# Kernel tuning notes

Measured on AMD Instinct MI355X. Metric: run time of the kernel, lower is better.

Reference implementation:

```python
import jax, jax.numpy as jnp
import numpy as np

N_NODES = 20000
N_EDGES = 320000
EMB = 128


def setup_inputs() -> dict:
    key = jax.random.key(0)
    ks = jax.random.split(key, 8)
    h = jax.random.normal(ks[0], (N_NODES, EMB), dtype=jnp.float32)
    W1 = jax.random.normal(ks[1], (2 * EMB, 4 * EMB), dtype=jnp.float32) / np.sqrt(2 * EMB)
    b1 = jnp.zeros((4 * EMB,), dtype=jnp.float32)
    W2 = jax.random.normal(ks[2], (4 * EMB, 1), dtype=jnp.float32) / np.sqrt(4 * EMB)
    b2 = jnp.zeros((1,), dtype=jnp.float32)
    # logistic-noise uniforms for RelaxedBernoulli rsample, kept away from {0,1}
    u = jax.random.uniform(ks[3], (N_EDGES,), dtype=jnp.float32, minval=1e-6, maxval=1.0 - 1e-6)
    row = jax.random.randint(ks[4], (N_EDGES,), 0, N_NODES, dtype=jnp.int32)
    col = jax.random.randint(ks[5], (N_EDGES,), 0, N_NODES, dtype=jnp.int32)
    edge_mask = -jnp.ones((N_EDGES,), dtype=jnp.int32)  # torch code initializes mask to -1
    return {"h": h, "W1": W1, "b1": b1, "W2": W2, "b2": b2,
            "u": u, "row": row, "col": col, "edge_mask": edge_mask, "hierarchy": 0}


def _segment_softmax(scores, seg, num_segments):
    m = jax.ops.segment_max(scores, seg, num_segments=num_segments)
    e = jnp.exp(scores - m[seg])
    s = jax.ops.segment_sum(e, seg, num_segments=num_segments)
    return e / s[seg]


TEMPERATURE = 1.0
RATIO = 0.5  # threshold for hard bernoulli


def reference(h, W1, b1, W2, b2, u, row, col, edge_mask, hierarchy):
    # edge gather + concat: [E, 2*EMB]
    edge_rep = jnp.concatenate([h[row], h[col]], axis=-1)
    # 2-layer MLP edge scorer -> [E]
    hid = jax.nn.relu(edge_rep @ W1 + b1)
    scores = (hid @ W2 + b2).reshape(-1)
    # segment softmax over edges grouped by source node (torch: softmax(edge_score, edge_index[0]))
    probs = _segment_softmax(scores, row, N_NODES)
    # RelaxedBernoulli(temperature, probs).rsample(): sigmoid((logits + logistic)/T)
    logits = jnp.log(probs) - jnp.log1p(-probs)
    logistic = jnp.log(u) - jnp.log1p(-u)
    y = jax.nn.sigmoid((logits + logistic) / TEMPERATURE)
    y_hard = (y > RATIO).astype(y.dtype)
    y_st = jax.lax.stop_gradient(y_hard - y) + y  # straight-through
    # edge_mask[y == 1] = hierarchy + 1
    new_mask = jnp.where(y_st == 1.0, jnp.int32(hierarchy + 1), edge_mask)
    c_idx = new_mask > 0
    s_idx = new_mask == -1
    causal_w = jnp.where(c_idx, scores, 0.0)
    spu_w = jnp.where(s_idx, -scores, 0.0)
    return scores, y_st, new_mask, causal_w, spu_w
```

## Files before the change

kernel.cpp:

```cpp
#include <hip/hip_runtime.h>
#include <math.h>

#define N_NODES 20000
#define N_EDGES 320000
#define EMB 128
#define HID 512
#define NCHUNK ((N_NODES + 1023) / 1024)

#define RPW 4
#define WPB 2
#define RPB (RPW * WPB)
#define FE_BLOCKS ((N_NODES + RPB - 1) / RPB)

typedef float v2f __attribute__((ext_vector_type(2)));

#if defined(__has_builtin)
#if __has_builtin(__builtin_elementwise_fma)
#define V2FMA(a, b, c) __builtin_elementwise_fma((a), (b), (c))
#else
#define V2FMA(a, b, c) ((a) * (b) + (c))
#endif
#else
#define V2FMA(a, b, c) ((a) * (b) + (c))
#endif

__global__ void init_deg(int* __restrict__ deg, int* __restrict__ offs) {
    int i = blockIdx.x * 256 + threadIdx.x;
    if (i < N_NODES) deg[i] = 0;
    if (i == 0) offs[N_NODES] = N_EDGES;
}

#define TM 128
#define TN 128
#define BK 8
#define NTILES (EMB / BK)
#define GEMM_MT ((N_NODES + TM - 1) / TM)
#define GEMM_BLOCKS (8 * GEMM_MT)
#define HIST_BLOCKS ((N_EDGES + 255) / 256)

__global__ __launch_bounds__(256) void gemm_hist(
    const float* __restrict__ h, const float* __restrict__ W1,
    const float* __restrict__ b1, float* __restrict__ P, float* __restrict__ Q,
    const int* __restrict__ row, int* __restrict__ deg)
{
    const int bid = blockIdx.x;
    const int tid = threadIdx.x;

    if (bid >= GEMM_BLOCKS) {
        const int e = (bid - GEMM_BLOCKS) * 256 + tid;
        if (e < N_EDGES) atomicAdd(&deg[row[e]], 1);
        return;
    }

    __shared__ float As[2][BK][TM + 4];
    __shared__ float Bs[2][BK][TN];

    const int nt = bid & 7;
    const int mt = bid >> 3;
    const int m_base = mt * TM;

    const int a_m = tid >> 1;
    const int a_k = (tid & 1) << 2;
    const int  row_a = m_base + a_m;
    const bool a_ok  = row_a < N_NODES;
    const float* __restrict__ hrow = h + (size_t)row_a * EMB + a_k;

    const int b_k = tid >> 5;
    const int b_n = (tid & 31) << 2;
    const int w_row_off = (nt < 4) ? 0 : 128;
    const int w_col     = (nt & 3) * TN + b_n;
    const float* __restrict__ wrow = W1 + (size_t)(w_row_off + b_k) * HID + w_col;

    const int ty = tid >> 4, tx = tid & 15;
    const int cm = ty << 2, cn = tx << 2;

    v2f acc[8][4] = {};

    float4 pa, pb;
    pa = make_float4(0.f, 0.f, 0.f, 0.f);
    if (a_ok) pa = *(const float4*)(hrow);
    pb = *(const float4*)(wrow);
    As[0][a_k + 0][a_m] = pa.x;
    As[0][a_k + 1][a_m] = pa.y;
    As[0][a_k + 2][a_m] = pa.z;
    As[0][a_k + 3][a_m] = pa.w;
    *(float4*)&Bs[0][b_k][b_n] = pb;
    __syncthreads();

    for (int t = 0; t < NTILES; ++t) {
        const int cur = t & 1;
        if (t + 1 < NTILES) {
            const int k0 = (t + 1) * BK;
            pa = make_float4(0.f, 0.f, 0.f, 0.f);
            if (a_ok) pa = *(const float4*)(hrow + k0);
            pb = *(const float4*)(wrow + (size_t)k0 * HID);
        }

#pragma unroll
        for (int kk = 0; kk < BK; ++kk) {
            float a[8];
            *(float4*)&a[0] = *(const float4*)&As[cur][kk][cm];
            *(float4*)&a[4] = *(const float4*)&As[cur][kk][cm + 64];
            float4 b0 = *(const float4*)&Bs[cur][kk][cn];
            float4 b1v = *(const float4*)&Bs[cur][kk][cn + 64];
            v2f bp[4] = {(v2f){b0.x, b0.y}, (v2f){b0.z, b0.w},
                         (v2f){b1v.x, b1v.y}, (v2f){b1v.z, b1v.w}};
#pragma unroll
            for (int i = 0; i < 8; ++i) {
                v2f ai = (v2f){a[i], a[i]};
#pragma unroll
                for (int j = 0; j < 4; ++j)
                    acc[i][j] = V2FMA(ai, bp[j], acc[i][j]);
            }
        }

        if (t + 1 < NTILES) {
            const int nxt = 1 - cur;
            As[nxt][a_k + 0][a_m] = pa.x;
            As[nxt][a_k + 1][a_m] = pa.y;
            As[nxt][a_k + 2][a_m] = pa.z;
            As[nxt][a_k + 3][a_m] = pa.w;
            *(float4*)&Bs[nxt][b_k][b_n] = pb;
            __syncthreads();
        }
    }

    const bool  isP = (nt < 4);
    const int   col_base = (nt & 3) * TN;
    float* __restrict__ dstbase = isP ? P : Q;

    v2f bias[4] = {{0.f,0.f},{0.f,0.f},{0.f,0.f},{0.f,0.f}};
    if (isP) {
        float4 bv0 = *(const float4*)(b1 + col_base + cn);
        float4 bv1 = *(const float4*)(b1 + col_base + cn + 64);
        bias[0] = (v2f){bv0.x, bv0.y};
        bias[1] = (v2f){bv0.z, bv0.w};
        bias[2] = (v2f){bv1.x, bv1.y};
        bias[3] = (v2f){bv1.z, bv1.w};
    }

#pragma unroll
    for (int i = 0; i < 8; ++i) {
        const int r = m_base + cm + (i < 4 ? i : 64 + i - 4);
        if (r < N_NODES) {
            float* dst = dstbase + (size_t)r * HID + col_base;
            v2f c0 = acc[i][0] + bias[0], c1 = acc[i][1] + bias[1];
            v2f c2 = acc[i][2] + bias[2], c3 = acc[i][3] + bias[3];
            *(float4*)(dst + cn)      = make_float4(c0.x, c0.y, c1.x, c1.y);
            *(float4*)(dst + cn + 64) = make_float4(c2.x, c2.y, c3.x, c3.y);
        }
    }
}

__device__ __forceinline__ int wave_incl_scan(int v, int lane) {
#pragma unroll
    for (int off = 1; off < 64; off <<= 1) {
        int t = __shfl_up(v, off, 64);
        if (lane >= off) v += t;
    }
    return v;
}

__global__ __launch_bounds__(1024) void scan_part(const int* __restrict__ deg,
                                                  int* __restrict__ part,
                                                  int* __restrict__ totals) {
    __shared__ int wsum[16];
    const int tid = threadIdx.x, lane = tid & 63, w = tid >> 6;
    const int i = blockIdx.x * 1024 + tid;
    int v = (i < N_NODES) ? deg[i] : 0;
    int incl = wave_incl_scan(v, lane);
    if (lane == 63) wsum[w] = incl;
    __syncthreads();
    if (w == 0) {
        int x = (lane < 16) ? wsum[lane] : 0;
        int xs = wave_incl_scan(x, lane);
        if (lane < 16) wsum[lane] = xs - x;
        if (lane == 15) totals[blockIdx.x] = xs;
    }
    __syncthreads();
    if (i < N_NODES) part[i] = wsum[w] + incl - v;
}

__global__ __launch_bounds__(1024) void scan_apply(const int* __restrict__ part,
                                                   const int* __restrict__ totals,
                                                   int* __restrict__ cursor,
                                                   int* __restrict__ offs) {
    __shared__ int carry_s;
    const int tid = threadIdx.x;
    if (tid < 64) {
        int v = (tid < NCHUNK) ? totals[tid] : 0;
        int incl = wave_incl_scan(v, tid);
        if (tid == (int)blockIdx.x) carry_s = incl - v;
    }
    __syncthreads();
    const int i = blockIdx.x * 1024 + tid;
    if (i < N_NODES) {
        int o = part[i] + carry_s;
        cursor[i] = o;
        offs[i] = o;
    }
}

__global__ void scatter_edges(const int* __restrict__ row, const int* __restrict__ col,
                              int* __restrict__ cursor,
                              unsigned short* __restrict__ cols16,
                              int* __restrict__ inv) {
    int e = blockIdx.x * 256 + threadIdx.x;
    if (e >= N_EDGES) return;
    int r = row[e];
    int pos = atomicAdd(&cursor[r], 1);
    cols16[pos] = (unsigned short)col[e];
    inv[e] = pos;
}

__device__ __forceinline__ float dot8_relu(const float4 qa, const float4 qb,
                                           const float4 p0, const float4 p1,
                                           const float4 w0, const float4 w1) {
    float t = 0.0f;
    t = fmaf(fmaxf(p0.x + qa.x, 0.0f), w0.x, t);
    t = fmaf(fmaxf(p0.y + qa.y, 0.0f), w0.y, t);
    t = fmaf(fmaxf(p0.z + qa.z, 0.0f), w0.z, t);
    t = fmaf(fmaxf(p0.w + qa.w, 0.0f), w0.w, t);
    t = fmaf(fmaxf(p1.x + qb.x, 0.0f), w1.x, t);
    t = fmaf(fmaxf(p1.y + qb.y, 0.0f), w1.y, t);
    t = fmaf(fmaxf(p1.z + qb.z, 0.0f), w1.z, t);
    t = fmaf(fmaxf(p1.w + qb.w, 0.0f), w1.w, t);
    return t;
}

__device__ __forceinline__ float chunk_scores(
    const float* __restrict__ Q, const unsigned short* __restrict__ cols16,
    int es_base, int nch, int lane, int j0,
    const float4 p0, const float4 p1, const float4 w0, const float4 w1,
    float bias2)
{
    int mycol = 0;
    if (lane < nch) mycol = (int)cols16[es_base + lane];
    float mysc = -INFINITY;

#define QL2(k, bb, d0, d1) { \
        int c_ = __shfl(mycol, (bb) + (k), 64); \
        const float* __restrict__ q_ = Q + (size_t)c_ * HID; \
        d0 = *(const float4*)(q_ + j0); \
        d1 = *(const float4*)(q_ + 256 + j0); }

    float4 a00, a01, a10, a11;
    QL2(0, 0, a00, a01); QL2(1, 0, a10, a11);

    for (int b = 0; b < nch; b += 2) {
        float4 n00, n01, n10, n11;
        const bool more = (b + 2) < nch;
        if (more) { QL2(0, b + 2, n00, n01); QL2(1, b + 2, n10, n11); }

        float s0 = dot8_relu(a00, a01, p0, p1, w0, w1);
        float s1 = dot8_relu(a10, a11, p0, p1, w0, w1);

#pragma unroll
        for (int off = 32; off > 0; off >>= 1) {
            s0 += __shfl_xor(s0, off, 64);
            s1 += __shfl_xor(s1, off, 64);
        }

        const int k = lane - b;
        if ((unsigned)k < 2u && lane < nch) mysc = (k ? s1 : s0) + bias2;

        if (more) { a00 = n00; a01 = n01; a10 = n10; a11 = n11; }
    }
#undef QL2
    return mysc;
}

__global__ __launch_bounds__(128) void fused_edge(
    const float* __restrict__ P, const float* __restrict__ Q,
    const float* __restrict__ W2, const float* __restrict__ b2,
    const unsigned short* __restrict__ cols16, const int* __restrict__ offs,
    float2* __restrict__ tmp)
{
    const int tid = threadIdx.x, lane = tid & 63, w = tid >> 6;
    const int r0 = blockIdx.x * RPB + w * RPW;
    const int r1 = (r0 + RPW < N_NODES) ? r0 + RPW : N_NODES;
    const int j0 = lane << 2;

    const float4 w0 = *(const float4*)(W2 + j0);
    const float4 w1 = *(const float4*)(W2 + 256 + j0);
    const float bias2 = b2[0];

    for (int r = r0; r < r1; ++r) {
        const int es = offs[r], ee = offs[r + 1];
        const int d = ee - es;
        if (d == 0) continue;

        const float* __restrict__ prow = P + (size_t)r * HID;
        const float4 p0 = *(const float4*)(prow + j0);
        const float4 p1 = *(const float4*)(prow + 256 + j0);

        if (d <= 64) {
            float mysc = chunk_scores(Q, cols16, es, d, lane, j0,
                                      p0, p1, w0, w1, bias2);

            float m = mysc;
#pragma unroll
            for (int off = 32; off > 0; off >>= 1)
                m = fmaxf(m, __shfl_xor(m, off, 64));

            float ev = (lane < d) ? expf(mysc - m) : 0.0f;
            float ssum = ev;
#pragma unroll
            for (int off = 32; off > 0; off >>= 1)
                ssum += __shfl_xor(ssum, off, 64);

            if (lane < d) {
                float p = ev / ssum;
                float logits = logf(p) - log1pf(-p);
                tmp[es + lane] = make_float2(mysc, logits);
            }
        } else {
            for (int base = 0; base < d; base += 64) {
                const int nch = (d - base < 64) ? d - base : 64;
                float mysc = chunk_scores(Q, cols16, es + base, nch, lane, j0,
                                          p0, p1, w0, w1, bias2);
                if (lane < nch) tmp[es + base + lane].x = mysc;
            }

            float m = -INFINITY;
            for (int j = lane; j < d; j += 64)
                m = fmaxf(m, tmp[es + j].x);
#pragma unroll
            for (int off = 32; off > 0; off >>= 1)
                m = fmaxf(m, __shfl_xor(m, off, 64));

            float ssum = 0.0f;
            for (int j = lane; j < d; j += 64)
                ssum += expf(tmp[es + j].x - m);
#pragma unroll
            for (int off = 32; off > 0; off >>= 1)
                ssum += __shfl_xor(ssum, off, 64);

            for (int j = lane; j < d; j += 64) {
                float s = tmp[es + j].x;
                float p = expf(s - m) / ssum;
                float logits = logf(p) - log1pf(-p);
                tmp[es + j] = make_float2(s, logits);
            }
        }
    }
}

__global__ __launch_bounds__(256) void unperm(
    const float2* __restrict__ tmp, const int* __restrict__ inv,
    const float* __restrict__ u, const int* __restrict__ edge_mask,
    const int* __restrict__ hierarchy,
    float* __restrict__ scores, float* __restrict__ out_y,
    float* __restrict__ out_mask, float* __restrict__ out_causal,
    float* __restrict__ out_spu)
{
    const int e = blockIdx.x * 256 + threadIdx.x;
    if (e >= N_EDGES) return;
    const float2 t = tmp[inv[e]];
    const float s = t.x;
    const float uu = u[e];
    const float L = logf(uu) - log1pf(-uu);
    const float y = 1.0f / (1.0f + expf(-(t.y + L)));
    const bool hard = y > 0.5f;
    const int mm = hard ? (hierarchy[0] + 1) : edge_mask[e];
    scores[e]     = s;
    out_y[e]      = hard ? 1.0f : 0.0f;
    out_mask[e]   = (float)mm;
    out_causal[e] = (mm > 0)   ?  s : 0.0f;
    out_spu[e]    = (mm == -1) ? -s : 0.0f;
}

extern "C" void kernel_launch(void* const* d_in, const int* in_sizes, int n_in,
                              void* d_out, int out_size, void* d_ws, size_t ws_size,
                              hipStream_t stream) {
    const float* h_ptr = (const float*)d_in[0];
    const float* W1    = (const float*)d_in[1];
    const float* b1    = (const float*)d_in[2];
    const float* W2    = (const float*)d_in[3];
    const float* b2    = (const float*)d_in[4];
    const float* u     = (const float*)d_in[5];
    const int*   row   = (const int*)d_in[6];
    const int*   col   = (const int*)d_in[7];
    const int*   emask = (const int*)d_in[8];
    const int*   hier  = (const int*)d_in[9];

    float* out        = (float*)d_out;
    float* scores     = out;
    float* out_y      = out + (size_t)N_EDGES;
    float* out_mask   = out + 2 * (size_t)N_EDGES;
    float* out_causal = out + 3 * (size_t)N_EDGES;
    float* out_spu    = out + 4 * (size_t)N_EDGES;

    float*          P      = (float*)d_ws;
    float*          Qm     = P + (size_t)N_NODES * HID;
    float2*         tmp    = (float2*)(Qm + (size_t)N_NODES * HID);
    unsigned short* cols16 = (unsigned short*)(tmp + N_EDGES);
    int*            inv    = (int*)(cols16 + N_EDGES);
    int*            deg    = inv + N_EDGES;
    int*            cursor = deg + N_NODES;
    int*            offs   = cursor + N_NODES;
    int*            part   = offs + N_NODES + 1;
    int*            totals = part + N_NODES;

    hipLaunchKernelGGL(init_deg, dim3((N_NODES + 255) / 256), dim3(256), 0, stream,
                       deg, offs);

    hipLaunchKernelGGL(gemm_hist, dim3(GEMM_BLOCKS + HIST_BLOCKS), dim3(256), 0, stream,
                       h_ptr, W1, b1, P, Qm, row, deg);

    hipLaunchKernelGGL(scan_part, dim3(NCHUNK), dim3(1024), 0, stream, deg, part, totals);
    hipLaunchKernelGGL(scan_apply, dim3(NCHUNK), dim3(1024), 0, stream,
                       part, totals, cursor, offs);
    hipLaunchKernelGGL(scatter_edges, dim3((N_EDGES + 255) / 256), dim3(256), 0, stream,
                       row, col, cursor, cols16, inv);

    hipLaunchKernelGGL(fused_edge, dim3(FE_BLOCKS), dim3(128), 0, stream,
                       P, Qm, W2, b2, cols16, offs, tmp);

    hipLaunchKernelGGL(unperm, dim3((N_EDGES + 255) / 256), dim3(256), 0, stream,
                       tmp, inv, u, emask, hier,
                       scores, out_y, out_mask, out_causal, out_spu);
}
```

Baseline: 275.6 us.

## Stream Q rows through an LDS ring via async global_load_lds across rows

Replaces the register double-buffered per-row chunk_scores with a per-wave 4-slot LDS ring filled by global_load_lds. Prefetches run continuously across the wave's rows instead of restarting at each row. Waits are handled with manual s_waitcnt vmcnt counts, and edges are scored one per iteration instead of two. The aim is to hide Q-gather latency across row boundaries. The risks are correctness of the hand-tuned vmcnt accounting, given other outstanding loads such as P and cols16, and lower instruction-level parallelism per iteration.

Measured after the change: 316.7 us. 14.9% more time.

```diff
diff --git a/kernel.cpp b/kernel.cpp
--- a/kernel.cpp
+++ b/kernel.cpp
@@ -11,6 +11,7 @@
 #define WPB 2
 #define RPB (RPW * WPB)
 #define FE_BLOCKS ((N_NODES + RPB - 1) / RPB)
+#define SLOTS 4
 
 typedef float v2f __attribute__((ext_vector_type(2)));
 
@@ -23,6 +24,14 @@
 #else
 #define V2FMA(a, b, c) ((a) * (b) + (c))
 #endif
+
+#define WAITVM(N) asm volatile("s_waitcnt vmcnt(" #N ")" ::: "memory")
+
+__device__ __forceinline__ void stage16(const float* g, float* l) {
+    __builtin_amdgcn_global_load_lds(
+        (const __attribute__((address_space(1))) void*)g,
+        (__attribute__((address_space(3))) void*)l, 16, 0, 0);
+}
 
 __global__ void init_deg(int* __restrict__ deg, int* __restrict__ offs) {
     int i = blockIdx.x * 256 + threadIdx.x;
@@ -135,6 +144,8 @@
         float4 bv1 = *(const float4*)(b1 + col_base + cn + 64);
         bias[0] = (v2f){bv0.x, bv0.y};
         bias[1] = (v2f){bv0.z, bv0.w};
+        bias[2] = (v2f){bv1.x, bv1.y};
+        bias[3] = (v2f){bv1.w == bv1.w ? bv1.x : bv1.x, bv1.y};
         bias[2] = (v2f){bv1.x, bv1.y};
         bias[3] = (v2f){bv1.z, bv1.w};
     }
@@ -228,76 +239,102 @@
     return t;
 }
 
-__device__ __forceinline__ float chunk_scores(
-    const float* __restrict__ Q, const unsigned short* __restrict__ cols16,
-    int es_base, int nch, int lane, int j0,
-    const float4 p0, const float4 p1, const float4 w0, const float4 w1,
-    float bias2)
-{
-    int mycol = 0;
-    if (lane < nch) mycol = (int)cols16[es_base + lane];
-    float mysc = -INFINITY;
-
-#define QL2(k, bb, d0, d1) { \
-        int c_ = __shfl(mycol, (bb) + (k), 64); \
-        const float* __restrict__ q_ = Q + (size_t)c_ * HID; \
-        d0 = *(const float4*)(q_ + j0); \
-        d1 = *(const float4*)(q_ + 256 + j0); }
-
-    float4 a00, a01, a10, a11;
-    QL2(0, 0, a00, a01); QL2(1, 0, a10, a11);
-
-    for (int b = 0; b < nch; b += 2) {
-        float4 n00, n01, n10, n11;
-        const bool more = (b + 2) < nch;
-        if (more) { QL2(0, b + 2, n00, n01); QL2(1, b + 2, n10, n11); }
-
-        float s0 = dot8_relu(a00, a01, p0, p1, w0, w1);
-        float s1 = dot8_relu(a10, a11, p0, p1, w0, w1);
-
-#pragma unroll
-        for (int off = 32; off > 0; off >>= 1) {
-            s0 += __shfl_xor(s0, off, 64);
-            s1 += __shfl_xor(s1, off, 64);
-        }
-
-        const int k = lane - b;
-        if ((unsigned)k < 2u && lane < nch) mysc = (k ? s1 : s0) + bias2;
-
-        if (more) { a00 = n00; a01 = n01; a10 = n10; a11 = n11; }
-    }
-#undef QL2
-    return mysc;
-}
-
 __global__ __launch_bounds__(128) void fused_edge(
     const float* __restrict__ P, const float* __restrict__ Q,
     const float* __restrict__ W2, const float* __restrict__ b2,
     const unsigned short* __restrict__ cols16, const int* __restrict__ offs,
     float2* __restrict__ tmp)
 {
+    __shared__ float ring[WPB][SLOTS][HID];
+
     const int tid = threadIdx.x, lane = tid & 63, w = tid >> 6;
     const int r0 = blockIdx.x * RPB + w * RPW;
-    const int r1 = (r0 + RPW < N_NODES) ? r0 + RPW : N_NODES;
+    if (r0 >= N_NODES) return;
+    const int nrow = (r0 + RPW <= N_NODES) ? RPW : (N_NODES - r0);
     const int j0 = lane << 2;
+
+    int o[RPW + 1];
+#pragma unroll
+    for (int t = 0; t <= RPW; ++t)
+        o[t] = offs[r0 + ((t <= nrow) ? t : nrow)];
+
+    const int es0 = o[0];
+    const int n = o[nrow] - es0;
+    if (n == 0) return;
 
     const float4 w0 = *(const float4*)(W2 + j0);
     const float4 w1 = *(const float4*)(W2 + 256 + j0);
     const float bias2 = b2[0];
 
-    for (int r = r0; r < r1; ++r) {
-        const int es = offs[r], ee = offs[r + 1];
-        const int d = ee - es;
+    int cb = 0;
+    int mc0 = 0, mc1 = 0;
+    if (lane < n) mc0 = (int)cols16[es0 + lane];
+    if (n > 64 && 64 + lane < n) mc1 = (int)cols16[es0 + 64 + lane];
+
+    const int pro = (n < SLOTS) ? n : SLOTS;
+    for (int jj = 0; jj < pro; ++jj) {
+        int c = __shfl(mc0, jj, 64);
+        const float* qs = Q + (size_t)c * HID;
+        stage16(qs + j0,       &ring[w][jj][0]);
+        stage16(qs + 256 + j0, &ring[w][jj][256]);
+    }
+
+    int i = 0;
+    for (int rr = 0; rr < nrow; ++rr) {
+        const int d = o[rr + 1] - o[rr];
         if (d == 0) continue;
-
+        const int r = r0 + rr;
         const float* __restrict__ prow = P + (size_t)r * HID;
         const float4 p0 = *(const float4*)(prow + j0);
         const float4 p1 = *(const float4*)(prow + 256 + j0);
 
+        const int es_r = es0 + i;
+        float mysc = -INFINITY;
+
+        for (int k = 0; k < d; ++k, ++i) {
+            if ((i >> 6) > cb) {
+                cb++;
+                mc0 = mc1;
+                mc1 = 0;
+                const int base = (cb + 1) << 6;
+                if (base < n && base + lane < n)
+                    mc1 = (int)cols16[es0 + base + lane];
+            }
+
+            const int rem = n - 1 - i;
+            if (rem >= 3)      { WAITVM(6); }
+            else if (rem == 2) { WAITVM(4); }
+            else if (rem == 1) { WAITVM(2); }
+            else               { WAITVM(0); }
+
+            const int sl = i & (SLOTS - 1);
+            const float4 q0 = *(const float4*)&ring[w][sl][j0];
+            const float4 q1 = *(const float4*)&ring[w][sl][256 + j0];
+
+            float s = dot8_relu(q0, q1, p0, p1, w0, w1);
+#pragma unroll
+            for (int off = 32; off > 0; off >>= 1)
+                s += __shfl_xor(s, off, 64);
+            const int kk = k & 63;
+            if (lane == kk) mysc = s + bias2;
+
+            if (kk == 63 && k != d - 1) {
+                tmp[es_r + (k - 63) + lane].x = mysc;
+                mysc = -INFINITY;
+            }
+
+            const int j = i + SLOTS;
+            if (j < n) {
+                const int mcsel = ((j >> 6) == cb) ? mc0 : mc1;
+                const int c = __shfl(mcsel, j & 63, 64);
+                const float* qs = Q + (size_t)c * HID;
+                const int s2 = j & (SLOTS - 1);
+                stage16(qs + j0,       &ring[w][s2][0]);
+                stage16(qs + 256 + j0, &ring[w][s2][256]);
+            }
+        }
+
         if (d <= 64) {
-            float mysc = chunk_scores(Q, cols16, es, d, lane, j0,
-                                      p0, p1, w0, w1, bias2);
-
             float m = mysc;
 #pragma unroll
             for (int off = 32; off > 0; off >>= 1)
@@ -312,35 +349,32 @@
             if (lane < d) {
                 float p = ev / ssum;
                 float logits = logf(p) - log1pf(-p);
-                tmp[es + lane] = make_float2(mysc, logits);
+                tmp[es_r + lane] = make_float2(mysc, logits);
             }
         } else {
-            for (int base = 0; base < d; base += 64) {
-                const int nch = (d - base < 64) ? d - base : 64;
-                float mysc = chunk_scores(Q, cols16, es + base, nch, lane, j0,
-                                          p0, p1, w0, w1, bias2);
-                if (lane < nch) tmp[es + base + lane].x = mysc;
-            }
+            const int last_base = ((d - 1) >> 6) << 6;
+            const int cnt = d - last_base;
+            if (lane < cnt) tmp[es_r + last_base + lane].x = mysc;
 
             float m = -INFINITY;
-            for (int j = lane; j < d; j += 64)
-                m = fmaxf(m, tmp[es + j].x);
+            for (int jj = lane; jj < d; jj += 64)
+                m = fmaxf(m, tmp[es_r + jj].x);
 #pragma unroll
             for (int off = 32; off > 0; off >>= 1)
                 m = fmaxf(m, __shfl_xor(m, off, 64));
 
             float ssum = 0.0f;
-            for (int j = lane; j < d; j += 64)
-                ssum += expf(tmp[es + j].x - m);
+            for (int jj = lane; jj < d; jj += 64)
+                ssum += expf(tmp[es_r + jj].x - m);
 #pragma unroll
             for (int off = 32; off > 0; off >>= 1)
                 ssum += __shfl_xor(ssum, off, 64);
 
-            for (int j = lane; j < d; j += 64) {
-                float s = tmp[es + j].x;
-                float p = expf(s - m) / ssum;
+            for (int jj = lane; jj < d; jj += 64) {
+                float sv = tmp[es_r + jj].x;
+                float p = expf(sv - m) / ssum;
                 float logits = logf(p) - log1pf(-p);
-                tmp[es + j] = make_float2(s, logits);
+                tmp[es_r + jj] = make_float2(sv, logits);
             }
         }
     }
```

## Replace FP32 FMA node GEMM with split-bf16 MFMA matrix-core GEMM

Applied to the files above, without the earlier changes.

Converts h and W1 into three-term bf16 splits in a prep kernel that also runs the degree histogram. A new GEMM then computes the P/Q node projections with 16x16x32 bf16 MFMA instructions, using six cross products to approximate FP32 accuracy. The goal is to move the per-node projection GEMM from vector FMA units onto matrix cores. In exchange it adds an extra kernel launch, writes and reads the bf16 split buffers, loads operands straight from global memory with no LDS tiling, and carries a small precision risk from dropping the lower-order split terms.

Result: slower. 330.1 us (+19.8%).

```diff
diff --git a/kernel.cpp b/kernel.cpp
--- a/kernel.cpp
+++ b/kernel.cpp
@@ -12,17 +12,19 @@
 #define RPB (RPW * WPB)
 #define FE_BLOCKS ((N_NODES + RPB - 1) / RPB)
 
-typedef float v2f __attribute__((ext_vector_type(2)));
-
-#if defined(__has_builtin)
-#if __has_builtin(__builtin_elementwise_fma)
-#define V2FMA(a, b, c) __builtin_elementwise_fma((a), (b), (c))
-#else
-#define V2FMA(a, b, c) ((a) * (b) + (c))
-#endif
-#else
-#define V2FMA(a, b, c) ((a) * (b) + (c))
-#endif
+#define GEMM_MT ((N_NODES + 127) / 128)
+#define GEMM_MFMA_BLOCKS (GEMM_MT * 8)
+
+#define PREP_H_BLOCKS 2500
+#define PREP_W_BLOCKS 512
+#define HIST_BLOCKS ((N_EDGES + 255) / 256)
+#define PREP_HIST_OFF (PREP_H_BLOCKS + PREP_W_BLOCKS)
+#define PREP_BLOCKS (PREP_HIST_OFF + HIST_BLOCKS)
+
+typedef __attribute__((ext_vector_type(8))) short bf16x8;
+typedef __attribute__((ext_vector_type(4))) float f32x4;
+
+#define MFMA16(a, b, c) __builtin_amdgcn_mfma_f32_16x16x32_bf16((a), (b), (c), 0, 0, 0)
 
 __global__ void init_deg(int* __restrict__ deg, int* __restrict__ offs) {
     int i = blockIdx.x * 256 + threadIdx.x;
@@ -30,124 +32,139 @@
     if (i == 0) offs[N_NODES] = N_EDGES;
 }
 
-#define TM 128
-#define TN 128
-#define BK 8
-#define NTILES (EMB / BK)
-#define GEMM_MT ((N_NODES + TM - 1) / TM)
-#define GEMM_BLOCKS (8 * GEMM_MT)
-#define HIST_BLOCKS ((N_EDGES + 255) / 256)
-
-__global__ __launch_bounds__(256) void gemm_hist(
+__device__ __forceinline__ unsigned short bf16rn(float x) {
+    unsigned u = __builtin_bit_cast(unsigned, x);
+    u += 0x7FFFu + ((u >> 16) & 1u);
+    return (unsigned short)(u >> 16);
+}
+__device__ __forceinline__ float bf2f(unsigned short b) {
+    unsigned u = ((unsigned)b) << 16;
+    return __builtin_bit_cast(float, u);
+}
+__device__ __forceinline__ void split3(float x, unsigned short& s1,
+                                       unsigned short& s2, unsigned short& s3) {
+    s1 = bf16rn(x);
+    float r = x - bf2f(s1);
+    s2 = bf16rn(r);
+    float r2 = r - bf2f(s2);
+    s3 = bf16rn(r2);
+}
+
+__global__ __launch_bounds__(256) void prep_hist(
     const float* __restrict__ h, const float* __restrict__ W1,
-    const float* __restrict__ b1, float* __restrict__ P, float* __restrict__ Q,
+    unsigned short* __restrict__ hs1, unsigned short* __restrict__ hs2,
+    unsigned short* __restrict__ hs3,
+    unsigned short* __restrict__ wt1, unsigned short* __restrict__ wt2,
+    unsigned short* __restrict__ wt3,
     const int* __restrict__ row, int* __restrict__ deg)
 {
+    const int bid = blockIdx.x, tid = threadIdx.x;
+
+    if (bid < PREP_H_BLOCKS) {
+        const int i4 = bid * 256 + tid;
+        const float4 v = ((const float4*)h)[i4];
+        unsigned short a1[4], a2[4], a3[4];
+        split3(v.x, a1[0], a2[0], a3[0]);
+        split3(v.y, a1[1], a2[1], a3[1]);
+        split3(v.z, a1[2], a2[2], a3[2]);
+        split3(v.w, a1[3], a2[3], a3[3]);
+#define PACK4(dst, a) { \
+            uint2 pk; \
+            pk.x = (unsigned)a[0] | ((unsigned)a[1] << 16); \
+            pk.y = (unsigned)a[2] | ((unsigned)a[3] << 16); \
+            *(uint2*)((dst) + (size_t)i4 * 4) = pk; }
+        PACK4(hs1, a1); PACK4(hs2, a2); PACK4(hs3, a3);
+#undef PACK4
+        return;
+    }
+
+    if (bid < PREP_HIST_OFF) {
+        const int t = (bid - PREP_H_BLOCKS) * 256 + tid;
+        const int k = t & 127, n = t >> 7;
+        const float x = W1[(size_t)(((n >> 9) << 7) + k) * HID + (n & 511)];
+        unsigned short s1, s2, s3;
+        split3(x, s1, s2, s3);
+        wt1[t] = s1; wt2[t] = s2; wt3[t] = s3;
+        return;
+    }
+
+    const int e = (bid - PREP_HIST_OFF) * 256 + tid;
+    if (e < N_EDGES) atomicAdd(&deg[row[e]], 1);
+}
+
+__global__ __launch_bounds__(256) void gemm_mfma(
+    const unsigned short* __restrict__ hs1, const unsigned short* __restrict__ hs2,
+    const unsigned short* __restrict__ hs3,
+    const unsigned short* __restrict__ wt1, const unsigned short* __restrict__ wt2,
+    const unsigned short* __restrict__ wt3,
+    const float* __restrict__ b1, float* __restrict__ P, float* __restrict__ Q)
+{
     const int bid = blockIdx.x;
-    const int tid = threadIdx.x;
-
-    if (bid >= GEMM_BLOCKS) {
-        const int e = (bid - GEMM_BLOCKS) * 256 + tid;
-        if (e < N_EDGES) atomicAdd(&deg[row[e]], 1);
-        return;
-    }
-
-    __shared__ float As[2][BK][TM + 4];
-    __shared__ float Bs[2][BK][TN];
-
-    const int nt = bid & 7;
-    const int mt = bid >> 3;
-    const int m_base = mt * TM;
-
-    const int a_m = tid >> 1;
-    const int a_k = (tid & 1) << 2;
-    const int  row_a = m_base + a_m;
-    const bool a_ok  = row_a < N_NODES;
-    const float* __restrict__ hrow = h + (size_t)row_a * EMB + a_k;
-
-    const int b_k = tid >> 5;
-    const int b_n = (tid & 31) << 2;
-    const int w_row_off = (nt < 4) ? 0 : 128;
-    const int w_col     = (nt & 3) * TN + b_n;
-    const float* __restrict__ wrow = W1 + (size_t)(w_row_off + b_k) * HID + w_col;
-
-    const int ty = tid >> 4, tx = tid & 15;
-    const int cm = ty << 2, cn = tx << 2;
-
-    v2f acc[8][4] = {};
-
-    float4 pa, pb;
-    pa = make_float4(0.f, 0.f, 0.f, 0.f);
-    if (a_ok) pa = *(const float4*)(hrow);
-    pb = *(const float4*)(wrow);
-    As[0][a_k + 0][a_m] = pa.x;
-    As[0][a_k + 1][a_m] = pa.y;
-    As[0][a_k + 2][a_m] = pa.z;
-    As[0][a_k + 3][a_m] = pa.w;
-    *(float4*)&Bs[0][b_k][b_n] = pb;
-    __syncthreads();
-
-    for (int t = 0; t < NTILES; ++t) {
-        const int cur = t & 1;
-        if (t + 1 < NTILES) {
-            const int k0 = (t + 1) * BK;
-            pa = make_float4(0.f, 0.f, 0.f, 0.f);
-            if (a_ok) pa = *(const float4*)(hrow + k0);
-            pb = *(const float4*)(wrow + (size_t)k0 * HID);
+    const int nt = bid & 7, mt = bid >> 3;
+    const int m_base = mt * 128;
+    const int tid = threadIdx.x, lane = tid & 63, w = tid >> 6;
+    const int l15 = lane & 15, l4 = lane >> 4;
+
+    int ar0 = m_base + w * 32 + l15;
+    int ar1 = ar0 + 16;
+    if (ar0 > N_NODES - 1) ar0 = N_NODES - 1;
+    if (ar1 > N_NODES - 1) ar1 = N_NODES - 1;
+    const size_t ao0 = (size_t)ar0 * 128 + l4 * 8;
+    const size_t ao1 = (size_t)ar1 * 128 + l4 * 8;
+    const size_t bo  = (size_t)(nt * 128 + l15) * 128 + l4 * 8;
+
+    f32x4 acc[2][8];
+#pragma unroll
+    for (int m = 0; m < 2; ++m)
+#pragma unroll
+        for (int n = 0; n < 8; ++n) acc[m][n] = (f32x4){0.f, 0.f, 0.f, 0.f};
+
+#pragma unroll
+    for (int ks = 0; ks < 4; ++ks) {
+        const int ko = ks * 32;
+        const bf16x8 a10 = *(const bf16x8*)(hs1 + ao0 + ko);
+        const bf16x8 a20 = *(const bf16x8*)(hs2 + ao0 + ko);
+        const bf16x8 a30 = *(const bf16x8*)(hs3 + ao0 + ko);
+        const bf16x8 a11 = *(const bf16x8*)(hs1 + ao1 + ko);
+        const bf16x8 a21 = *(const bf16x8*)(hs2 + ao1 + ko);
+        const bf16x8 a31 = *(const bf16x8*)(hs3 + ao1 + ko);
+#pragma unroll
+        for (int n0 = 0; n0 < 8; ++n0) {
+            const int off = n0 * 2048 + ko;
+            const bf16x8 bv1 = *(const bf16x8*)(wt1 + bo + off);
+            const bf16x8 bv2 = *(const bf16x8*)(wt2 + bo + off);
+            const bf16x8 bv3 = *(const bf16x8*)(wt3 + bo + off);
+            acc[0][n0] = MFMA16(a10, bv1, acc[0][n0]);
+            acc[0][n0] = MFMA16(a10, bv2, acc[0][n0]);
+            acc[0][n0] = MFMA16(a20, bv1, acc[0][n0]);
+            acc[0][n0] = MFMA16(a20, bv2, acc[0][n0]);
+            acc[0][n0] = MFMA16(a10, bv3, acc[0][n0]);
+            acc[0][n0] = MFMA16(a30, bv1, acc[0][n0]);
+            acc[1][n0] = MFMA16(a11, bv1, acc[1][n0]);
+            acc[1][n0] = MFMA16(a11, bv2, acc[1][n0]);
+            acc[1][n0] = MFMA16(a21, bv1, acc[1][n0]);
+            acc[1][n0] = MFMA16(a21, bv2, acc[1][n0]);
+            acc[1][n0] = MFMA16(a11, bv3, acc[1][n0]);
+            acc[1][n0] = MFMA16(a31, bv1, acc[1][n0]);
         }
-
-#pragma unroll
-        for (int kk = 0; kk < BK; ++kk) {
-            float a[8];
-            *(float4*)&a[0] = *(const float4*)&As[cur][kk][cm];
-            *(float4*)&a[4] = *(const float4*)&As[cur][kk][cm + 64];
-            float4 b0 = *(const float4*)&Bs[cur][kk][cn];
-            float4 b1v = *(const float4*)&Bs[cur][kk][cn + 64];
-            v2f bp[4] = {(v2f){b0.x, b0.y}, (v2f){b0.z, b0.w},
-                         (v2f){b1v.x, b1v.y}, (v2f){b1v.z, b1v.w}};
-#pragma unroll
-            for (int i = 0; i < 8; ++i) {
-                v2f ai = (v2f){a[i], a[i]};
-#pragma unroll
-                for (int j = 0; j < 4; ++j)
-                    acc[i][j] = V2FMA(ai, bp[j], acc[i][j]);
+    }
+
+    const bool isP = nt < 4;
+    float* __restrict__ dst = isP ? P : Q;
+    const int colb = (nt & 3) * 128;
+#pragma unroll
+    for (int n0 = 0; n0 < 8; ++n0) {
+        const int col = colb + n0 * 16 + l15;
+        const float bias = isP ? b1[col] : 0.0f;
+#pragma unroll
+        for (int m = 0; m < 2; ++m) {
+            const int rbase = m_base + w * 32 + m * 16 + l4 * 4;
+#pragma unroll
+            for (int r = 0; r < 4; ++r) {
+                const int rr = rbase + r;
+                if (rr < N_NODES)
+                    dst[(size_t)rr * HID + col] = acc[m][n0][r] + bias;
             }
-        }
-
-        if (t + 1 < NTILES) {
-            const int nxt = 1 - cur;
-            As[nxt][a_k + 0][a_m] = pa.x;
-            As[nxt][a_k + 1][a_m] = pa.y;
-            As[nxt][a_k + 2][a_m] = pa.z;
-            As[nxt][a_k + 3][a_m] = pa.w;
-            *(float4*)&Bs[nxt][b_k][b_n] = pb;
-            __syncthreads();
-        }
-    }
-
-    const bool  isP = (nt < 4);
-    const int   col_base = (nt & 3) * TN;
-    float* __restrict__ dstbase = isP ? P : Q;
-
-    v2f bias[4] = {{0.f,0.f},{0.f,0.f},{0.f,0.f},{0.f,0.f}};
-    if (isP) {
-        float4 bv0 = *(const float4*)(b1 + col_base + cn);
-        float4 bv1 = *(const float4*)(b1 + col_base + cn + 64);
-        bias[0] = (v2f){bv0.x, bv0.y};
-        bias[1] = (v2f){bv0.z, bv0.w};
-        bias[2] = (v2f){bv1.x, bv1.y};
-        bias[3] = (v2f){bv1.z, bv1.w};
-    }
-
-#pragma unroll
-    for (int i = 0; i < 8; ++i) {
-        const int r = m_base + cm + (i < 4 ? i : 64 + i - 4);
-        if (r < N_NODES) {
-            float* dst = dstbase + (size_t)r * HID + col_base;
-            v2f c0 = acc[i][0] + bias[0], c1 = acc[i][1] + bias[1];
-            v2f c2 = acc[i][2] + bias[2], c3 = acc[i][3] + bias[3];
-            *(float4*)(dst + cn)      = make_float4(c0.x, c0.y, c1.x, c1.y);
-            *(float4*)(dst + cn + 64) = make_float4(c2.x, c2.y, c3.x, c3.y);
         }
     }
 }
@@ -393,20 +410,29 @@
 
     float*          P      = (float*)d_ws;
     float*          Qm     = P + (size_t)N_NODES * HID;
-    float2*         tmp    = (float2*)(Qm + (size_t)N_NODES * HID);
-    unsigned short* cols16 = (unsigned short*)(tmp + N_EDGES);
-    int*            inv    = (int*)(cols16 + N_EDGES);
-    int*            deg    = inv + N_EDGES;
+    unsigned short* hs1    = (unsigned short*)(Qm + (size_t)N_NODES * HID);
+    unsigned short* hs2    = hs1 + (size_t)N_NODES * EMB;
+    unsigned short* hs3    = hs2 + (size_t)N_NODES * EMB;
+    unsigned short* wt1    = hs3 + (size_t)N_NODES * EMB;
+    unsigned short* wt2    = wt1 + 1024 * 128;
+    unsigned short* wt3    = wt2 + 1024 * 128;
+    int*            deg    = (int*)(wt3 + 1024 * 128);
     int*            cursor = deg + N_NODES;
     int*            offs   = cursor + N_NODES;
     int*            part   = offs + N_NODES + 1;
     int*            totals = part + N_NODES;
+    float2*         tmp    = (float2*)hs1;
+    unsigned short* cols16 = (unsigned short*)(tmp + N_EDGES);
+    int*            inv    = (int*)(cols16 + N_EDGES);
 
     hipLaunchKernelGGL(init_deg, dim3((N_NODES + 255) / 256), dim3(256), 0, stream,
                        deg, offs);
 
-    hipLaunchKernelGGL(gemm_hist, dim3(GEMM_BLOCKS + HIST_BLOCKS), dim3(256), 0, stream,
-                       h_ptr, W1, b1, P, Qm, row, deg);
+    hipLaunchKernelGGL(prep_hist, dim3(PREP_BLOCKS), dim3(256), 0, stream,
+                       h_ptr, W1, hs1, hs2, hs3, wt1, wt2, wt3, row, deg);
+
+    hipLaunchKernelGGL(gemm_mfma, dim3(GEMM_MFMA_BLOCKS), dim3(256), 0, stream,
+                       hs1, hs2, hs3, wt1, wt2, wt3, b1, P, Qm);
 
     hipLaunchKernelGGL(scan_part, dim3(NCHUNK), dim3(1024), 0, stream, deg, part, totals);
     hipLaunchKernelGGL(scan_apply, dim3(NCHUNK), dim3(1024), 0, stream,
```
